# Kernel optimization log

Measured on AMD Instinct MI355X. Metric: run time of the kernel, lower is better.

Reference implementation:

```python
import math
import jax, jax.numpy as jnp
import numpy as np

NUM_HEADS = 8
ATTN_STD = [1.0] * 8                 # per-head gaussian std (broadcast from len-1 config)
ATTN_OFFSET = [-3, -2, -1, 0, 0, 1, 2, 3]  # per-head positional offset
ATTN_THRESHOLD = -1.0                # <=0 means no thresholding
WORD_COUNT_RATIO = 1.0


def gaussian_attn(qlen, vlen, dtype=jnp.float32):
    """Hard-coded positional attention weights, [H, qlen, vlen].
    Equivalent to get_attn_cache + offset-shifted fancy indexing:
    w[h,q,v] = N(v - offset_h - q*ratio; 0, std_h) pdf value."""
    std = jnp.asarray(ATTN_STD, jnp.float32)[:, None, None]
    ofs = jnp.asarray(ATTN_OFFSET, jnp.float32)[:, None, None]
    q = jnp.arange(qlen, dtype=jnp.float32)[None, :, None] * WORD_COUNT_RATIO
    v = jnp.arange(vlen, dtype=jnp.float32)[None, None, :]
    diff = (v - ofs) - q
    logits = jnp.exp(-0.5 * (diff / std) ** 2) / (std * math.sqrt(2.0 * math.pi))
    if ATTN_THRESHOLD > 0:
        logits = jnp.where(logits < ATTN_THRESHOLD, 0.0, logits)
    return logits.astype(dtype)


def setup_inputs() -> dict:
    key = jax.random.key(0)
    k0, k1, k2, k3 = jax.random.split(key, 4)
    B, L, E = 8, 1024, 1024
    values = jax.random.normal(k0, (B, L, E), jnp.float32)
    queries = jax.random.normal(k1, (B, L, E), jnp.float32)
    key_mask = jnp.zeros((B, L), dtype=bool)
    # xavier-ish scale for linear weights
    input_weights = jax.random.normal(k2, (E, E), jnp.float32) * (1.0 / math.sqrt(E))
    output_weight = jax.random.normal(k3, (E, E), jnp.float32) * (1.0 / math.sqrt(E))
    return {"values": values, "queries": queries, "key_mask": key_mask,
            "input_weights": input_weights, "output_weight": output_weight}


def reference(values, queries, key_mask, input_weights, output_weight):
    B, Lv, E = values.shape
    Lq = queries.shape[1]
    H = NUM_HEADS
    d = E // H
    # value projection (F.linear: x @ W.T), split into heads: [B, H, Lv, d]
    v = (values @ input_weights.T).reshape(B, Lv, H, d).transpose(0, 2, 1, 3)
    # masked_fill_ on padded key positions
    v = jnp.where(key_mask[:, None, :, None], 0.0, v)
    attn = gaussian_attn(Lq, Lv)                     # [H, Lq, Lv] shared over batch
    attended = jnp.einsum('hqv,bhvd->bhqd', attn, v)  # [B, H, Lq, d]
    out = attended.transpose(0, 2, 1, 3).reshape(B, Lq, E)  # mha_reshape
    return out @ output_weight.T                     # output_projection (no bias)
```

## Files before the change

kernel.cpp:

```cpp
#include <hip/hip_runtime.h>
#include <hip/hip_bf16.h>
#include <cstddef>


#define BATCH 8
#define SEQL  1024
#define EMB   1024
#define VROWS 1032

typedef unsigned short u16;
typedef __attribute__((ext_vector_type(8))) short s16x8;
typedef __attribute__((ext_vector_type(4))) float f32x4;
typedef __attribute__((ext_vector_type(8))) unsigned short u16x8;
typedef __attribute__((ext_vector_type(4))) unsigned short u16x4;

#define GLOAD_LDS16(g, l)                                                     \
    __builtin_amdgcn_global_load_lds(                                         \
        (const __attribute__((address_space(1))) void*)(g),                   \
        (__attribute__((address_space(3))) void*)(l), 16, 0, 0)

__device__ __forceinline__ u16 f2bf(float f) {
    unsigned u = __builtin_bit_cast(unsigned, f);
    u += 0x7FFF + ((u >> 16) & 1);
    return (u16)(u >> 16);
}

__constant__ float c_w[9] = {
    1.3383022576488537e-04f, 4.431848411938008e-03f, 5.399096651318806e-02f,
    2.4197072451914337e-01f, 3.989422804014327e-01f, 2.4197072451914337e-01f,
    5.399096651318806e-02f,  4.431848411938008e-03f, 1.3383022576488537e-04f
};
__constant__ int c_ofs[8] = { -3, -2, -1, 0, 0, 1, 2, 3 };

__global__ __launch_bounds__(256) void smooth_direct8(
    const float* __restrict__ values, const unsigned char* __restrict__ mask,
    const float* __restrict__ wi, const float* __restrict__ wo,
    u16* __restrict__ VG, u16* __restrict__ wib, u16* __restrict__ wob)
{
    const int blk = blockIdx.x;
    const int NS = BATCH * (VROWS / 8);
    if (blk < NS) {
        const int b  = blk & 7;
        const int g  = blk >> 3;
        const int r0 = g * 8;
        const int c  = threadIdx.x * 4;
        const float* vb = values + (size_t)b * SEQL * EMB + c;
        const unsigned char* mrow = mask + b * SEQL;

        f32x4 acc[8] = {};
        #pragma unroll
        for (int i = 0; i < 16; ++i) {
            const int v  = r0 - 8 + i;
            const int vc = v < 0 ? 0 : (v > SEQL - 1 ? SEQL - 1 : v);
            const float f = ((unsigned)v < (unsigned)SEQL && !mrow[vc]) ? 1.f : 0.f;
            const float4 x = *(const float4*)(vb + (size_t)vc * EMB);
            const float x0 = x.x * f, x1 = x.y * f, x2 = x.z * f, x3 = x.w * f;
            #pragma unroll
            for (int k = 0; k < 8; ++k) {
                const int j = i - k;
                if (j < 0 || j > 8) continue;
                const float w = c_w[j];
                acc[k][0] = fmaf(w, x0, acc[k][0]);
                acc[k][1] = fmaf(w, x1, acc[k][1]);
                acc[k][2] = fmaf(w, x2, acc[k][2]);
                acc[k][3] = fmaf(w, x3, acc[k][3]);
            }
        }
        u16* og = VG + (size_t)(b * VROWS + r0) * EMB + c;
        #pragma unroll
        for (int k = 0; k < 8; ++k) {
            u16x4 o;
            o[0] = f2bf(acc[k][0]); o[1] = f2bf(acc[k][1]);
            o[2] = f2bf(acc[k][2]); o[3] = f2bf(acc[k][3]);
            *(u16x4*)(og + (size_t)k * EMB) = o;
        }
    } else {
        const int k = (blk - NS) * 256 + threadIdx.x;
        const float* src = (k < 131072) ? wi : wo;
        u16* dst = (k < 131072) ? wib : wob;
        const size_t off = (size_t)(k & 131071) * 8;
        const float4 a = *(const float4*)(src + off);
        const float4 b4 = *(const float4*)(src + off + 4);
        u16x8 o;
        o[0] = f2bf(a.x);  o[1] = f2bf(a.y);  o[2] = f2bf(a.z);  o[3] = f2bf(a.w);
        o[4] = f2bf(b4.x); o[5] = f2bf(b4.y); o[6] = f2bf(b4.z); o[7] = f2bf(b4.w);
        *(u16x8*)(dst + off) = o;
    }
}

constexpr int BM = 256, BN = 128, BK = 64;
constexpr int A_EL = BM * BK;
constexpr int B_EL = BN * BK;
constexpr int BUF_EL = A_EL + B_EL;

template <bool OUT_BF16, bool SHIFTED>
__global__ __launch_bounds__(512, 2) void gemm_nt_pipe(
    const u16* __restrict__ A, const u16* __restrict__ B,
    void* __restrict__ Cout, int M, int N, int K)
{
    __shared__ u16 lds[3 * BUF_EL];

    const int tid  = threadIdx.x;
    const int lane = tid & 63;
    const int wave = tid >> 6;

    const int nwg = gridDim.x;
    const int bid = blockIdx.x;
    const int swz = (bid & 7) * (nwg >> 3) + (bid >> 3);
    const int ntn = N >> 7;
    const int row0 = (swz / ntn) * BM;
    const int col0 = (swz % ntn) * BN;

    int arow0;
    if (SHIFTED) {
        const int b  = row0 >> 10;
        const int q0 = row0 & (SEQL - 1);
        arow0 = b * VROWS + q0 + 4 + c_ofs[col0 >> 7];
    } else {
        arow0 = row0;
    }
    const u16* Ab = A + (size_t)arow0 * K;
    const u16* Bb = B + (size_t)col0 * K;

    const int wm = wave >> 1;
    const int wn = wave & 1;
    const int fr = lane & 15;
    const int fg = lane >> 4;

    const int srow   = tid >> 3;
    const int schunk = tid & 7;

    f32x4 acc[4][4] = {};
    s16x8 af[4][2], bf0[2][2], bf1[2][2];

    auto stageA3 = [&](int bsel, int kt) {
        u16* Abuf = lds + bsel * BUF_EL;
        const int k0 = kt << 6;
        #pragma unroll
        for (int c = 0; c < 3; ++c) {
            const int row = c * 64 + srow;
            const int sc  = (schunk ^ (row & 7)) << 3;
            GLOAD_LDS16(Ab + (size_t)row * K + k0 + sc, Abuf + c * 4096 + wave * 512);
        }
    };
    auto stageRest = [&](int bsel, int kt) {
        u16* Abuf = lds + bsel * BUF_EL;
        u16* Bbuf = Abuf + A_EL;
        const int k0 = kt << 6;
        {
            const int row = 192 + srow;
            const int sc  = (schunk ^ (row & 7)) << 3;
            GLOAD_LDS16(Ab + (size_t)row * K + k0 + sc, Abuf + 3 * 4096 + wave * 512);
        }
        #pragma unroll
        for (int c = 0; c < 2; ++c) {
            const int row = c * 64 + srow;
            const int sc  = (schunk ^ (row & 7)) << 3;
            GLOAD_LDS16(Bb + (size_t)row * K + k0 + sc, Bbuf + c * 4096 + wave * 512);
        }
    };

    auto phase0 = [&](int tile, bool doStage) {
        const u16* Abuf = lds + (tile % 3) * BUF_EL;
        const u16* Bbuf = Abuf + A_EL;
        #pragma unroll
        for (int m = 0; m < 4; ++m)
            #pragma unroll
            for (int kk = 0; kk < 2; ++kk) {
                const int row = wm * 64 + m * 16 + fr;
                const int ch  = ((kk << 2) + fg) ^ (row & 7);
                af[m][kk] = *(const s16x8*)(Abuf + row * 64 + ch * 8);
            }
        #pragma unroll
        for (int n = 0; n < 2; ++n)
            #pragma unroll
            for (int kk = 0; kk < 2; ++kk) {
                const int row = wn * 64 + n * 16 + fr;
                const int ch  = ((kk << 2) + fg) ^ (row & 7);
                bf0[n][kk] = *(const s16x8*)(Bbuf + row * 64 + ch * 8);
            }
        if (doStage) stageA3((tile + 2) % 3, tile + 2);
        __builtin_amdgcn_s_barrier();
        asm volatile("s_waitcnt lgkmcnt(0)" ::: "memory");
        __builtin_amdgcn_sched_barrier(0);
        __builtin_amdgcn_s_setprio(1);
        #pragma unroll
        for (int m = 0; m < 4; ++m)
            #pragma unroll
            for (int n = 0; n < 2; ++n)
                #pragma unroll
                for (int kk = 0; kk < 2; ++kk)
                    acc[m][n] = __builtin_amdgcn_mfma_f32_16x16x32_bf16(
                        af[m][kk], bf0[n][kk], acc[m][n], 0, 0, 0);
        __builtin_amdgcn_s_setprio(0);
        __builtin_amdgcn_s_barrier();
    };

    auto phase1 = [&](int tile, int mode ) {
        const u16* Abuf = lds + (tile % 3) * BUF_EL;
        const u16* Bbuf = Abuf + A_EL;
        #pragma unroll
        for (int n = 0; n < 2; ++n)
            #pragma unroll
            for (int kk = 0; kk < 2; ++kk) {
                const int row = wn * 64 + (2 + n) * 16 + fr;
                const int ch  = ((kk << 2) + fg) ^ (row & 7);
                bf1[n][kk] = *(const s16x8*)(Bbuf + row * 64 + ch * 8);
            }
        if (mode == 0) {
            stageRest((tile + 2) % 3, tile + 2);
            asm volatile("s_waitcnt vmcnt(6)" ::: "memory");
        } else if (mode == 1) {
            asm volatile("s_waitcnt vmcnt(0)" ::: "memory");
        }
        __builtin_amdgcn_s_barrier();
        asm volatile("s_waitcnt lgkmcnt(0)" ::: "memory");
        __builtin_amdgcn_sched_barrier(0);
        __builtin_amdgcn_s_setprio(1);
        #pragma unroll
        for (int m = 0; m < 4; ++m)
            #pragma unroll
            for (int n = 0; n < 2; ++n)
                #pragma unroll
                for (int kk = 0; kk < 2; ++kk)
                    acc[m][2 + n] = __builtin_amdgcn_mfma_f32_16x16x32_bf16(
                        af[m][kk], bf1[n][kk], acc[m][2 + n], 0, 0, 0);
        __builtin_amdgcn_s_setprio(0);
        __builtin_amdgcn_s_barrier();
    };

    const int NT = K >> 6;

    stageA3(0, 0); stageRest(0, 0);
    stageA3(1, 1); stageRest(1, 1);
    asm volatile("s_waitcnt vmcnt(6)" ::: "memory");
    __builtin_amdgcn_s_barrier();

    for (int t = 0; t < NT - 2; ++t) { phase0(t, true); phase1(t, 0); }
    phase0(NT - 2, false); phase1(NT - 2, 1);
    phase0(NT - 1, false); phase1(NT - 1, 2);

    const int crow0 = row0 + wm * 64 + fg * 4;
    const int ccol0 = col0 + wn * 64 + fr;
    if (OUT_BF16) {
        u16* C = (u16*)Cout;
        #pragma unroll
        for (int m = 0; m < 4; ++m)
            #pragma unroll
            for (int n = 0; n < 4; ++n)
                #pragma unroll
                for (int j = 0; j < 4; ++j)
                    C[(size_t)(crow0 + m * 16 + j) * N + ccol0 + n * 16] =
                        f2bf(acc[m][n][j]);
    } else {
        float* C = (float*)Cout;
        #pragma unroll
        for (int m = 0; m < 4; ++m)
            #pragma unroll
            for (int n = 0; n < 4; ++n)
                #pragma unroll
                for (int j = 0; j < 4; ++j)
                    C[(size_t)(crow0 + m * 16 + j) * N + ccol0 + n * 16] =
                        acc[m][n][j];
    }
}

extern "C" void kernel_launch(void* const* d_in, const int* in_sizes, int n_in,
                              void* d_out, int out_size, void* d_ws, size_t ws_size,
                              hipStream_t stream) {
    const float* values = (const float*)d_in[0];
    const unsigned char* mask = (const unsigned char*)d_in[2];
    const float* Win  = (const float*)d_in[3];
    const float* Wout = (const float*)d_in[4];
    float* out = (float*)d_out;

    const int M = BATCH * SEQL;
    const int N = EMB;
    const int K = EMB;

    u16* VG    = (u16*)d_ws;
    u16* Attb  = VG + (size_t)BATCH * VROWS * EMB;
    u16* Winb  = Attb + (size_t)M * EMB;
    u16* Woutb = Winb + (size_t)EMB * EMB;

    smooth_direct8<<<BATCH * (VROWS / 8) + 1024, 256, 0, stream>>>(
        values, mask, Win, Wout, VG, Winb, Woutb);

    dim3 ggrid((M / BM) * (N / BN));
    gemm_nt_pipe<true,  true ><<<ggrid, 512, 0, stream>>>(VG,   Winb,  Attb, M, N, K);
    gemm_nt_pipe<false, false><<<ggrid, 512, 0, stream>>>(Attb, Woutb, out,  M, N, K);
}
```

Before: 62.65 us.

## Split GEMM k-tile into four barrier phases and re-tile smoothing kernel

Result: slower. 66.27 us (+5.8%).

```diff
diff --git a/kernel.cpp b/kernel.cpp
--- a/kernel.cpp
+++ b/kernel.cpp
@@ -6,13 +6,12 @@
 #define BATCH 8
 #define SEQL  1024
 #define EMB   1024
-#define VROWS 1032
+#define VROWS 1040
 
 typedef unsigned short u16;
 typedef __attribute__((ext_vector_type(8))) short s16x8;
 typedef __attribute__((ext_vector_type(4))) float f32x4;
 typedef __attribute__((ext_vector_type(8))) unsigned short u16x8;
-typedef __attribute__((ext_vector_type(4))) unsigned short u16x4;
 
 #define GLOAD_LDS16(g, l)                                                     \
     __builtin_amdgcn_global_load_lds(                                         \
@@ -25,57 +24,66 @@
     return (u16)(u >> 16);
 }
 
-__constant__ float c_w[9] = {
-    1.3383022576488537e-04f, 4.431848411938008e-03f, 5.399096651318806e-02f,
-    2.4197072451914337e-01f, 3.989422804014327e-01f, 2.4197072451914337e-01f,
-    5.399096651318806e-02f,  4.431848411938008e-03f, 1.3383022576488537e-04f
-};
 __constant__ int c_ofs[8] = { -3, -2, -1, 0, 0, 1, 2, 3 };
 
-__global__ __launch_bounds__(256) void smooth_direct8(
+__global__ __launch_bounds__(256) void smooth16(
     const float* __restrict__ values, const unsigned char* __restrict__ mask,
     const float* __restrict__ wi, const float* __restrict__ wo,
     u16* __restrict__ VG, u16* __restrict__ wib, u16* __restrict__ wob)
 {
+    constexpr float W[9] = {
+        1.3383022576488537e-04f, 4.431848411938008e-03f, 5.399096651318806e-02f,
+        2.4197072451914337e-01f, 3.989422804014327e-01f, 2.4197072451914337e-01f,
+        5.399096651318806e-02f,  4.431848411938008e-03f, 1.3383022576488537e-04f
+    };
     const int blk = blockIdx.x;
-    const int NS = BATCH * (VROWS / 8);
-    if (blk < NS) {
-        const int b  = blk & 7;
-        const int g  = blk >> 3;
-        const int r0 = g * 8;
-        const int c  = threadIdx.x * 4;
-        const float* vb = values + (size_t)b * SEQL * EMB + c;
+    const int NSM = BATCH * (VROWS / 8);
+    if (blk < NSM) {
+        const int b   = blk & 7;
+        const int gg  = blk >> 3;
+        const int sub = threadIdx.x >> 7;
+        const int r0  = gg * 8 + sub * 4;
+        const int ct  = (threadIdx.x & 127) * 8;
+        const float* vb = values + (size_t)b * SEQL * EMB + ct;
         const unsigned char* mrow = mask + b * SEQL;
 
-        f32x4 acc[8] = {};
-        #pragma unroll
-        for (int i = 0; i < 16; ++i) {
+        f32x4 accA[4] = {}, accB[4] = {};
+        #pragma unroll
+        for (int i = 0; i < 12; ++i) {
             const int v  = r0 - 8 + i;
             const int vc = v < 0 ? 0 : (v > SEQL - 1 ? SEQL - 1 : v);
             const float f = ((unsigned)v < (unsigned)SEQL && !mrow[vc]) ? 1.f : 0.f;
-            const float4 x = *(const float4*)(vb + (size_t)vc * EMB);
-            const float x0 = x.x * f, x1 = x.y * f, x2 = x.z * f, x3 = x.w * f;
+            const float4 xA = *(const float4*)(vb + (size_t)vc * EMB);
+            const float4 xB = *(const float4*)(vb + (size_t)vc * EMB + 4);
+            const float a0 = xA.x * f, a1 = xA.y * f, a2 = xA.z * f, a3 = xA.w * f;
+            const float b0 = xB.x * f, b1 = xB.y * f, b2 = xB.z * f, b3 = xB.w * f;
             #pragma unroll
-            for (int k = 0; k < 8; ++k) {
+            for (int k = 0; k < 4; ++k) {
                 const int j = i - k;
                 if (j < 0 || j > 8) continue;
-                const float w = c_w[j];
-                acc[k][0] = fmaf(w, x0, acc[k][0]);
-                acc[k][1] = fmaf(w, x1, acc[k][1]);
-                acc[k][2] = fmaf(w, x2, acc[k][2]);
-                acc[k][3] = fmaf(w, x3, acc[k][3]);
+                const float w = W[j];
+                accA[k][0] = fmaf(w, a0, accA[k][0]);
+                accA[k][1] = fmaf(w, a1, accA[k][1]);
+                accA[k][2] = fmaf(w, a2, accA[k][2]);
+                accA[k][3] = fmaf(w, a3, accA[k][3]);
+                accB[k][0] = fmaf(w, b0, accB[k][0]);
+                accB[k][1] = fmaf(w, b1, accB[k][1]);
+                accB[k][2] = fmaf(w, b2, accB[k][2]);
+                accB[k][3] = fmaf(w, b3, accB[k][3]);
             }
         }
-        u16* og = VG + (size_t)(b * VROWS + r0) * EMB + c;
-        #pragma unroll
-        for (int k = 0; k < 8; ++k) {
-            u16x4 o;
-            o[0] = f2bf(acc[k][0]); o[1] = f2bf(acc[k][1]);
-            o[2] = f2bf(acc[k][2]); o[3] = f2bf(acc[k][3]);
-            *(u16x4*)(og + (size_t)k * EMB) = o;
+        u16* og = VG + (size_t)(b * VROWS + r0) * EMB + ct;
+        #pragma unroll
+        for (int k = 0; k < 4; ++k) {
+            u16x8 o;
+            o[0] = f2bf(accA[k][0]); o[1] = f2bf(accA[k][1]);
+            o[2] = f2bf(accA[k][2]); o[3] = f2bf(accA[k][3]);
+            o[4] = f2bf(accB[k][0]); o[5] = f2bf(accB[k][1]);
+            o[6] = f2bf(accB[k][2]); o[7] = f2bf(accB[k][3]);
+            *(u16x8*)(og + (size_t)k * EMB) = o;
         }
     } else {
-        const int k = (blk - NS) * 256 + threadIdx.x;
+        const int k = (blk - NSM) * 256 + threadIdx.x;
         const float* src = (k < 131072) ? wi : wo;
         u16* dst = (k < 131072) ? wib : wob;
         const size_t off = (size_t)(k & 131071) * 8;
@@ -131,7 +139,6 @@
     const int schunk = tid & 7;
 
     f32x4 acc[4][4] = {};
-    s16x8 af[4][2], bf0[2][2], bf1[2][2];
 
     auto stageA3 = [&](int bsel, int kt) {
         u16* Abuf = lds + bsel * BUF_EL;
@@ -160,73 +167,53 @@
         }
     };
 
-    auto phase0 = [&](int tile, bool doStage) {
+    auto doTile = [&](int tile, int mode) {
         const u16* Abuf = lds + (tile % 3) * BUF_EL;
         const u16* Bbuf = Abuf + A_EL;
-        #pragma unroll
-        for (int m = 0; m < 4; ++m)
-            #pragma unroll
-            for (int kk = 0; kk < 2; ++kk) {
-                const int row = wm * 64 + m * 16 + fr;
-                const int ch  = ((kk << 2) + fg) ^ (row & 7);
-                af[m][kk] = *(const s16x8*)(Abuf + row * 64 + ch * 8);
-            }
-        #pragma unroll
-        for (int n = 0; n < 2; ++n)
-            #pragma unroll
-            for (int kk = 0; kk < 2; ++kk) {
-                const int row = wn * 64 + n * 16 + fr;
-                const int ch  = ((kk << 2) + fg) ^ (row & 7);
-                bf0[n][kk] = *(const s16x8*)(Bbuf + row * 64 + ch * 8);
-            }
-        if (doStage) stageA3((tile + 2) % 3, tile + 2);
-        __builtin_amdgcn_s_barrier();
-        asm volatile("s_waitcnt lgkmcnt(0)" ::: "memory");
-        __builtin_amdgcn_sched_barrier(0);
-        __builtin_amdgcn_s_setprio(1);
-        #pragma unroll
-        for (int m = 0; m < 4; ++m)
-            #pragma unroll
-            for (int n = 0; n < 2; ++n)
-                #pragma unroll
-                for (int kk = 0; kk < 2; ++kk)
-                    acc[m][n] = __builtin_amdgcn_mfma_f32_16x16x32_bf16(
-                        af[m][kk], bf0[n][kk], acc[m][n], 0, 0, 0);
-        __builtin_amdgcn_s_setprio(0);
-        __builtin_amdgcn_s_barrier();
-    };
-
-    auto phase1 = [&](int tile, int mode ) {
-        const u16* Abuf = lds + (tile % 3) * BUF_EL;
-        const u16* Bbuf = Abuf + A_EL;
-        #pragma unroll
-        for (int n = 0; n < 2; ++n)
-            #pragma unroll
-            for (int kk = 0; kk < 2; ++kk) {
-                const int row = wn * 64 + (2 + n) * 16 + fr;
-                const int ch  = ((kk << 2) + fg) ^ (row & 7);
-                bf1[n][kk] = *(const s16x8*)(Bbuf + row * 64 + ch * 8);
-            }
-        if (mode == 0) {
-            stageRest((tile + 2) % 3, tile + 2);
-            asm volatile("s_waitcnt vmcnt(6)" ::: "memory");
-        } else if (mode == 1) {
-            asm volatile("s_waitcnt vmcnt(0)" ::: "memory");
-        }
-        __builtin_amdgcn_s_barrier();
-        asm volatile("s_waitcnt lgkmcnt(0)" ::: "memory");
-        __builtin_amdgcn_sched_barrier(0);
-        __builtin_amdgcn_s_setprio(1);
-        #pragma unroll
-        for (int m = 0; m < 4; ++m)
-            #pragma unroll
-            for (int n = 0; n < 2; ++n)
-                #pragma unroll
-                for (int kk = 0; kk < 2; ++kk)
-                    acc[m][2 + n] = __builtin_amdgcn_mfma_f32_16x16x32_bf16(
-                        af[m][kk], bf1[n][kk], acc[m][2 + n], 0, 0, 0);
-        __builtin_amdgcn_s_setprio(0);
-        __builtin_amdgcn_s_barrier();
+        s16x8 a0, a1, a2, a3, b0, b1;
+
+        auto rdA = [&](int kk) {
+            const int ch0 = ((kk << 2) + fg);
+            {const int r = wm*64 +  0 + fr; a0 = *(const s16x8*)(Abuf + r*64 + (ch0^(r&7))*8);}
+            {const int r = wm*64 + 16 + fr; a1 = *(const s16x8*)(Abuf + r*64 + (ch0^(r&7))*8);}
+            {const int r = wm*64 + 32 + fr; a2 = *(const s16x8*)(Abuf + r*64 + (ch0^(r&7))*8);}
+            {const int r = wm*64 + 48 + fr; a3 = *(const s16x8*)(Abuf + r*64 + (ch0^(r&7))*8);}
+        };
+        auto rdB = [&](int kk, int np) {
+            const int ch0 = ((kk << 2) + fg);
+            {const int r = wn*64 + (np*2+0)*16 + fr; b0 = *(const s16x8*)(Bbuf + r*64 + (ch0^(r&7))*8);}
+            {const int r = wn*64 + (np*2+1)*16 + fr; b1 = *(const s16x8*)(Bbuf + r*64 + (ch0^(r&7))*8);}
+        };
+        auto fire = [&](int n0) {
+            __builtin_amdgcn_s_setprio(1);
+            acc[0][n0  ] = __builtin_amdgcn_mfma_f32_16x16x32_bf16(a0, b0, acc[0][n0  ], 0, 0, 0);
+            acc[0][n0+1] = __builtin_amdgcn_mfma_f32_16x16x32_bf16(a0, b1, acc[0][n0+1], 0, 0, 0);
+            acc[1][n0  ] = __builtin_amdgcn_mfma_f32_16x16x32_bf16(a1, b0, acc[1][n0  ], 0, 0, 0);
+            acc[1][n0+1] = __builtin_amdgcn_mfma_f32_16x16x32_bf16(a1, b1, acc[1][n0+1], 0, 0, 0);
+            acc[2][n0  ] = __builtin_amdgcn_mfma_f32_16x16x32_bf16(a2, b0, acc[2][n0  ], 0, 0, 0);
+            acc[2][n0+1] = __builtin_amdgcn_mfma_f32_16x16x32_bf16(a2, b1, acc[2][n0+1], 0, 0, 0);
+            acc[3][n0  ] = __builtin_amdgcn_mfma_f32_16x16x32_bf16(a3, b0, acc[3][n0  ], 0, 0, 0);
+            acc[3][n0+1] = __builtin_amdgcn_mfma_f32_16x16x32_bf16(a3, b1, acc[3][n0+1], 0, 0, 0);
+            __builtin_amdgcn_s_setprio(0);
+        };
+        auto barrier_in = [&]() {
+            __builtin_amdgcn_s_barrier();
+            asm volatile("s_waitcnt lgkmcnt(0)" ::: "memory");
+            __builtin_amdgcn_sched_barrier(0);
+        };
+
+        rdA(0); rdB(0, 0);
+        if (mode == 0) stageA3((tile + 2) % 3, tile + 2);
+        barrier_in(); fire(0); __builtin_amdgcn_s_barrier();
+        rdB(0, 1);
+        if (mode == 0) stageRest((tile + 2) % 3, tile + 2);
+        barrier_in(); fire(2); __builtin_amdgcn_s_barrier();
+        rdA(1); rdB(1, 0);
+        barrier_in(); fire(0); __builtin_amdgcn_s_barrier();
+        rdB(1, 1);
+        if (mode == 0)      asm volatile("s_waitcnt vmcnt(6)" ::: "memory");
+        else if (mode == 1) asm volatile("s_waitcnt vmcnt(0)" ::: "memory");
+        barrier_in(); fire(2); __builtin_amdgcn_s_barrier();
     };
 
     const int NT = K >> 6;
@@ -236,9 +223,9 @@
     asm volatile("s_waitcnt vmcnt(6)" ::: "memory");
     __builtin_amdgcn_s_barrier();
 
-    for (int t = 0; t < NT - 2; ++t) { phase0(t, true); phase1(t, 0); }
-    phase0(NT - 2, false); phase1(NT - 2, 1);
-    phase0(NT - 1, false); phase1(NT - 1, 2);
+    for (int t = 0; t < NT - 2; ++t) doTile(t, 0);
+    doTile(NT - 2, 1);
+    doTile(NT - 1, 2);
 
     const int crow0 = row0 + wm * 64 + fg * 4;
     const int ccol0 = col0 + wn * 64 + fr;
@@ -283,7 +270,7 @@
     u16* Winb  = Attb + (size_t)M * EMB;
     u16* Woutb = Winb + (size_t)EMB * EMB;
 
-    smooth_direct8<<<BATCH * (VROWS / 8) + 1024, 256, 0, stream>>>(
+    smooth16<<<BATCH * (VROWS / 8) + 1024, 256, 0, stream>>>(
         values, mask, Win, Wout, VG, Winb, Woutb);
 
     dim3 ggrid((M / BM) * (N / BN));
```

## Fuse gaussian smoothing of values into first GEMM's A-tile staging

Applied to the files above, without the earlier changes.

Result: slower. 94.19 us (+50.3%).

```diff
diff --git a/kernel.cpp b/kernel.cpp
--- a/kernel.cpp
+++ b/kernel.cpp
@@ -6,7 +6,6 @@
 #define BATCH 8
 #define SEQL  1024
 #define EMB   1024
-#define VROWS 1032
 
 typedef unsigned short u16;
 typedef __attribute__((ext_vector_type(8))) short s16x8;
@@ -25,67 +24,22 @@
     return (u16)(u >> 16);
 }
 
-__constant__ float c_w[9] = {
-    1.3383022576488537e-04f, 4.431848411938008e-03f, 5.399096651318806e-02f,
-    2.4197072451914337e-01f, 3.989422804014327e-01f, 2.4197072451914337e-01f,
-    5.399096651318806e-02f,  4.431848411938008e-03f, 1.3383022576488537e-04f
-};
 __constant__ int c_ofs[8] = { -3, -2, -1, 0, 0, 1, 2, 3 };
 
-__global__ __launch_bounds__(256) void smooth_direct8(
-    const float* __restrict__ values, const unsigned char* __restrict__ mask,
+__global__ __launch_bounds__(256) void wcvt(
     const float* __restrict__ wi, const float* __restrict__ wo,
-    u16* __restrict__ VG, u16* __restrict__ wib, u16* __restrict__ wob)
+    u16* __restrict__ wib, u16* __restrict__ wob)
 {
-    const int blk = blockIdx.x;
-    const int NS = BATCH * (VROWS / 8);
-    if (blk < NS) {
-        const int b  = blk & 7;
-        const int g  = blk >> 3;
-        const int r0 = g * 8;
-        const int c  = threadIdx.x * 4;
-        const float* vb = values + (size_t)b * SEQL * EMB + c;
-        const unsigned char* mrow = mask + b * SEQL;
-
-        f32x4 acc[8] = {};
-        #pragma unroll
-        for (int i = 0; i < 16; ++i) {
-            const int v  = r0 - 8 + i;
-            const int vc = v < 0 ? 0 : (v > SEQL - 1 ? SEQL - 1 : v);
-            const float f = ((unsigned)v < (unsigned)SEQL && !mrow[vc]) ? 1.f : 0.f;
-            const float4 x = *(const float4*)(vb + (size_t)vc * EMB);
-            const float x0 = x.x * f, x1 = x.y * f, x2 = x.z * f, x3 = x.w * f;
-            #pragma unroll
-            for (int k = 0; k < 8; ++k) {
-                const int j = i - k;
-                if (j < 0 || j > 8) continue;
-                const float w = c_w[j];
-                acc[k][0] = fmaf(w, x0, acc[k][0]);
-                acc[k][1] = fmaf(w, x1, acc[k][1]);
-                acc[k][2] = fmaf(w, x2, acc[k][2]);
-                acc[k][3] = fmaf(w, x3, acc[k][3]);
-            }
-        }
-        u16* og = VG + (size_t)(b * VROWS + r0) * EMB + c;
-        #pragma unroll
-        for (int k = 0; k < 8; ++k) {
-            u16x4 o;
-            o[0] = f2bf(acc[k][0]); o[1] = f2bf(acc[k][1]);
-            o[2] = f2bf(acc[k][2]); o[3] = f2bf(acc[k][3]);
-            *(u16x4*)(og + (size_t)k * EMB) = o;
-        }
-    } else {
-        const int k = (blk - NS) * 256 + threadIdx.x;
-        const float* src = (k < 131072) ? wi : wo;
-        u16* dst = (k < 131072) ? wib : wob;
-        const size_t off = (size_t)(k & 131071) * 8;
-        const float4 a = *(const float4*)(src + off);
-        const float4 b4 = *(const float4*)(src + off + 4);
-        u16x8 o;
-        o[0] = f2bf(a.x);  o[1] = f2bf(a.y);  o[2] = f2bf(a.z);  o[3] = f2bf(a.w);
-        o[4] = f2bf(b4.x); o[5] = f2bf(b4.y); o[6] = f2bf(b4.z); o[7] = f2bf(b4.w);
-        *(u16x8*)(dst + off) = o;
-    }
+    const int k = blockIdx.x * 256 + threadIdx.x;
+    const float* src = (k < 131072) ? wi : wo;
+    u16* dst = (k < 131072) ? wib : wob;
+    const size_t off = (size_t)(k & 131071) * 8;
+    const float4 a = *(const float4*)(src + off);
+    const float4 b4 = *(const float4*)(src + off + 4);
+    u16x8 o;
+    o[0] = f2bf(a.x);  o[1] = f2bf(a.y);  o[2] = f2bf(a.z);  o[3] = f2bf(a.w);
+    o[4] = f2bf(b4.x); o[5] = f2bf(b4.y); o[6] = f2bf(b4.z); o[7] = f2bf(b4.w);
+    *(u16x8*)(dst + off) = o;
 }
 
 constexpr int BM = 256, BN = 128, BK = 64;
@@ -93,16 +47,21 @@
 constexpr int B_EL = BN * BK;
 constexpr int BUF_EL = A_EL + B_EL;
 
-template <bool OUT_BF16, bool SHIFTED>
-__global__ __launch_bounds__(512, 2) void gemm_nt_pipe(
-    const u16* __restrict__ A, const u16* __restrict__ B,
-    void* __restrict__ Cout, int M, int N, int K)
+__global__ __launch_bounds__(512, 2) void gemm1_smooth(
+    const float* __restrict__ values, const unsigned char* __restrict__ mask,
+    const u16* __restrict__ Bw, u16* __restrict__ Cout)
 {
+    constexpr float W[9] = {
+        1.3383022576488537e-04f, 4.431848411938008e-03f, 5.399096651318806e-02f,
+        2.4197072451914337e-01f, 3.989422804014327e-01f, 2.4197072451914337e-01f,
+        5.399096651318806e-02f,  4.431848411938008e-03f, 1.3383022576488537e-04f
+    };
     __shared__ u16 lds[3 * BUF_EL];
 
     const int tid  = threadIdx.x;
     const int lane = tid & 63;
     const int wave = tid >> 6;
+    const int K = EMB, N = EMB;
 
     const int nwg = gridDim.x;
     const int bid = blockIdx.x;
@@ -111,15 +70,196 @@
     const int row0 = (swz / ntn) * BM;
     const int col0 = (swz % ntn) * BN;
 
-    int arow0;
-    if (SHIFTED) {
-        const int b  = row0 >> 10;
-        const int q0 = row0 & (SEQL - 1);
-        arow0 = b * VROWS + q0 + 4 + c_ofs[col0 >> 7];
-    } else {
-        arow0 = row0;
+    const int b  = row0 >> 10;
+    const int q0 = row0 & (SEQL - 1);
+    const int rb = q0 + c_ofs[col0 >> 7];
+
+    const u16* Bb = Bw + (size_t)col0 * K;
+
+    const int wm = wave >> 1;
+    const int wn = wave & 1;
+    const int fr = lane & 15;
+    const int fg = lane >> 4;
+
+    const int srow   = tid >> 3;
+    const int schunk = tid & 7;
+
+    const int rowgrp = tid >> 4;
+    const int colgrp = tid & 15;
+    const int r0s = rowgrp * 8;
+    const float* vsrc = values + (size_t)b * SEQL * EMB + colgrp * 4;
+    const unsigned char* mrow = mask + b * SEQL;
+
+    int   voff[16];
+    float fH[16];
+    #pragma unroll
+    for (int i = 0; i < 16; ++i) {
+        const int praw = rb + r0s - 4 + i;
+        const int vc = praw < 0 ? 0 : (praw > SEQL - 1 ? SEQL - 1 : praw);
+        voff[i] = vc;
+        fH[i] = ((unsigned)praw < (unsigned)SEQL && !mrow[vc]) ? 1.f : 0.f;
     }
-    const u16* Ab = A + (size_t)arow0 * K;
+
+    f32x4 acc[4][4] = {};
+    f32x4 xr[16];
+    s16x8 af[4][2], bf0[2][2], bf1[2][2];
+
+    auto loadA = [&](int kt) {
+        const int k0 = kt << 6;
+        #pragma unroll
+        for (int i = 0; i < 16; ++i)
+            xr[i] = *(const f32x4*)(vsrc + (size_t)voff[i] * EMB + k0);
+    };
+    auto stageB = [&](int bsel, int kt) {
+        u16* Bdst = lds + bsel * BUF_EL + A_EL;
+        const int k0 = kt << 6;
+        #pragma unroll
+        for (int c = 0; c < 2; ++c) {
+            const int row = c * 64 + srow;
+            const int sc  = (schunk ^ (row & 7)) << 3;
+            GLOAD_LDS16(Bb + (size_t)row * K + k0 + sc, Bdst + c * 4096 + wave * 512);
+        }
+    };
+    auto smoothWrite = [&](int bsel) {
+        u16* Adst = lds + bsel * BUF_EL;
+        #pragma unroll
+        for (int i = 0; i < 16; ++i) {
+            xr[i][0] *= fH[i]; xr[i][1] *= fH[i];
+            xr[i][2] *= fH[i]; xr[i][3] *= fH[i];
+        }
+        #pragma unroll
+        for (int k = 0; k < 8; ++k) {
+            f32x4 s = {};
+            #pragma unroll
+            for (int j = 0; j < 9; ++j) {
+                const float w = W[j];
+                s[0] = fmaf(w, xr[k + j][0], s[0]);
+                s[1] = fmaf(w, xr[k + j][1], s[1]);
+                s[2] = fmaf(w, xr[k + j][2], s[2]);
+                s[3] = fmaf(w, xr[k + j][3], s[3]);
+            }
+            u16x4 o;
+            o[0] = f2bf(s[0]); o[1] = f2bf(s[1]); o[2] = f2bf(s[2]); o[3] = f2bf(s[3]);
+            const int rout = r0s + k;
+            const int slot = (colgrp >> 1) ^ (rout & 7);
+            *(u16x4*)(Adst + rout * 64 + slot * 8 + (colgrp & 1) * 4) = o;
+        }
+    };
+
+    auto phase0 = [&](int tile, bool doStage) {
+        const u16* Abuf = lds + (tile % 3) * BUF_EL;
+        const u16* Bbuf = Abuf + A_EL;
+        #pragma unroll
+        for (int m = 0; m < 4; ++m)
+            #pragma unroll
+            for (int kk = 0; kk < 2; ++kk) {
+                const int row = wm * 64 + m * 16 + fr;
+                const int ch  = ((kk << 2) + fg) ^ (row & 7);
+                af[m][kk] = *(const s16x8*)(Abuf + row * 64 + ch * 8);
+            }
+        #pragma unroll
+        for (int n = 0; n < 2; ++n)
+            #pragma unroll
+            for (int kk = 0; kk < 2; ++kk) {
+                const int row = wn * 64 + n * 16 + fr;
+                const int ch  = ((kk << 2) + fg) ^ (row & 7);
+                bf0[n][kk] = *(const s16x8*)(Bbuf + row * 64 + ch * 8);
+            }
+        if (doStage) { loadA(tile + 2); stageB((tile + 2) % 3, tile + 2); }
+        __builtin_amdgcn_s_barrier();
+        asm volatile("s_waitcnt lgkmcnt(0)" ::: "memory");
+        __builtin_amdgcn_sched_barrier(0);
+        __builtin_amdgcn_s_setprio(1);
+        #pragma unroll
+        for (int m = 0; m < 4; ++m)
+            #pragma unroll
+            for (int n = 0; n < 2; ++n)
+                #pragma unroll
+                for (int kk = 0; kk < 2; ++kk)
+                    acc[m][n] = __builtin_amdgcn_mfma_f32_16x16x32_bf16(
+                        af[m][kk], bf0[n][kk], acc[m][n], 0, 0, 0);
+        __builtin_amdgcn_s_setprio(0);
+        __builtin_amdgcn_s_barrier();
+    };
+
+    auto phase1 = [&](int tile, int mode ) {
+        const u16* Abuf = lds + (tile % 3) * BUF_EL;
+        const u16* Bbuf = Abuf + A_EL;
+        #pragma unroll
+        for (int n = 0; n < 2; ++n)
+            #pragma unroll
+            for (int kk = 0; kk < 2; ++kk) {
+                const int row = wn * 64 + (2 + n) * 16 + fr;
+                const int ch  = ((kk << 2) + fg) ^ (row & 7);
+                bf1[n][kk] = *(const s16x8*)(Bbuf + row * 64 + ch * 8);
+            }
+        if (mode == 0) {
+            smoothWrite((tile + 2) % 3);
+            asm volatile("s_waitcnt vmcnt(2)" ::: "memory");
+        } else if (mode == 1) {
+            asm volatile("s_waitcnt vmcnt(0)" ::: "memory");
+        }
+        __builtin_amdgcn_s_barrier();
+        asm volatile("s_waitcnt lgkmcnt(0)" ::: "memory");
+        __builtin_amdgcn_sched_barrier(0);
+        __builtin_amdgcn_s_setprio(1);
+        #pragma unroll
+        for (int m = 0; m < 4; ++m)
+            #pragma unroll
+            for (int n = 0; n < 2; ++n)
+                #pragma unroll
+                for (int kk = 0; kk < 2; ++kk)
+                    acc[m][2 + n] = __builtin_amdgcn_mfma_f32_16x16x32_bf16(
+                        af[m][kk], bf1[n][kk], acc[m][2 + n], 0, 0, 0);
+        __builtin_amdgcn_s_setprio(0);
+        __builtin_amdgcn_s_barrier();
+    };
+
+    const int NT = K >> 6;
+
+    loadA(0); stageB(0, 0);
+    smoothWrite(0);
+    loadA(1); stageB(1, 1);
+    smoothWrite(1);
+    asm volatile("s_waitcnt vmcnt(2)" ::: "memory");
+    asm volatile("s_waitcnt lgkmcnt(0)" ::: "memory");
+    __builtin_amdgcn_s_barrier();
+
+    for (int t = 0; t < NT - 2; ++t) { phase0(t, true); phase1(t, 0); }
+    phase0(NT - 2, false); phase1(NT - 2, 1);
+    phase0(NT - 1, false); phase1(NT - 1, 2);
+
+    const int crow0 = row0 + wm * 64 + fg * 4;
+    const int ccol0 = col0 + wn * 64 + fr;
+    u16* C = Cout;
+    #pragma unroll
+    for (int m = 0; m < 4; ++m)
+        #pragma unroll
+        for (int n = 0; n < 4; ++n)
+            #pragma unroll
+            for (int j = 0; j < 4; ++j)
+                C[(size_t)(crow0 + m * 16 + j) * N + ccol0 + n * 16] =
+                    f2bf(acc[m][n][j]);
+}
+
+__global__ __launch_bounds__(512, 2) void gemm_nt_pipe(
+    const u16* __restrict__ A, const u16* __restrict__ B,
+    float* __restrict__ Cout, int M, int N, int K)
+{
+    __shared__ u16 lds[3 * BUF_EL];
+
+    const int tid  = threadIdx.x;
+    const int lane = tid & 63;
+    const int wave = tid >> 6;
+
+    const int nwg = gridDim.x;
+    const int bid = blockIdx.x;
+    const int swz = (bid & 7) * (nwg >> 3) + (bid >> 3);
+    const int ntn = N >> 7;
+    const int row0 = (swz / ntn) * BM;
+    const int col0 = (swz % ntn) * BN;
+
+    const u16* Ab = A + (size_t)row0 * K;
     const u16* Bb = B + (size_t)col0 * K;
 
     const int wm = wave >> 1;
@@ -196,7 +336,7 @@
         __builtin_amdgcn_s_barrier();
     };
 
-    auto phase1 = [&](int tile, int mode ) {
+    auto phase1 = [&](int tile, int mode) {
         const u16* Abuf = lds + (tile % 3) * BUF_EL;
         const u16* Bbuf = Abuf + A_EL;
         #pragma unroll
@@ -242,27 +382,14 @@
 
     const int crow0 = row0 + wm * 64 + fg * 4;
     const int ccol0 = col0 + wn * 64 + fr;
-    if (OUT_BF16) {
-        u16* C = (u16*)Cout;
-        #pragma unroll
-        for (int m = 0; m < 4; ++m)
-            #pragma unroll
-            for (int n = 0; n < 4; ++n)
-                #pragma unroll
-                for (int j = 0; j < 4; ++j)
-                    C[(size_t)(crow0 + m * 16 + j) * N + ccol0 + n * 16] =
-                        f2bf(acc[m][n][j]);
-    } else {
-        float* C = (float*)Cout;
-        #pragma unroll
-        for (int m = 0; m < 4; ++m)
-            #pragma unroll
-            for (int n = 0; n < 4; ++n)
-                #pragma unroll
-                for (int j = 0; j < 4; ++j)
-                    C[(size_t)(crow0 + m * 16 + j) * N + ccol0 + n * 16] =
-                        acc[m][n][j];
-    }
+    #pragma unroll
+    for (int m = 0; m < 4; ++m)
+        #pragma unroll
+        for (int n = 0; n < 4; ++n)
+            #pragma unroll
+            for (int j = 0; j < 4; ++j)
+                Cout[(size_t)(crow0 + m * 16 + j) * N + ccol0 + n * 16] =
+                    acc[m][n][j];
 }
 
 extern "C" void kernel_launch(void* const* d_in, const int* in_sizes, int n_in,
@@ -278,15 +405,13 @@
     const int N = EMB;
     const int K = EMB;
 
-    u16* VG    = (u16*)d_ws;
-    u16* Attb  = VG + (size_t)BATCH * VROWS * EMB;
+    u16* Attb  = (u16*)d_ws;
     u16* Winb  = Attb + (size_t)M * EMB;
     u16* Woutb = Winb + (size_t)EMB * EMB;
 
-    smooth_direct8<<<BATCH * (VROWS / 8) + 1024, 256, 0, stream>>>(
-        values, mask, Win, Wout, VG, Winb, Woutb);
+    wcvt<<<1024, 256, 0, stream>>>(Win, Wout, Winb, Woutb);
 
     dim3 ggrid((M / BM) * (N / BN));
-    gemm_nt_pipe<true,  true ><<<ggrid, 512, 0, stream>>>(VG,   Winb,  Attb, M, N, K);
-    gemm_nt_pipe<false, false><<<ggrid, 512, 0, stream>>>(Attb, Woutb, out,  M, N, K);
+    gemm1_smooth<<<ggrid, 512, 0, stream>>>(values, mask, Winb, Attb);
+    gemm_nt_pipe<<<ggrid, 512, 0, stream>>>(Attb, Woutb, out, M, N, K);
 }
```
